# Optimization experiments

Measured on AMD Instinct MI355X. Metric: run time of the kernel, lower is better.

Reference implementation:

```python
import jax, jax.numpy as jnp
import numpy as np

EMBED_DIM = 512
NUM_HEADS = 8
HEAD_DIM = EMBED_DIM // NUM_HEADS
LN_EPS = 1e-5


def setup_inputs() -> dict:
    key = jax.random.key(0)
    ks = jax.random.split(key, 14)
    B, Lq, Lkv, E = 4, 1024, 4096, EMBED_DIM
    s = 0.02
    return {
        "query": jax.random.normal(ks[0], (B, Lq, E), dtype=jnp.float32),
        "key_value": jax.random.normal(ks[1], (B, Lkv, E), dtype=jnp.float32),
        "w_q": jax.random.normal(ks[2], (E, E), dtype=jnp.float32) * s,
        "w_k": jax.random.normal(ks[3], (E, E), dtype=jnp.float32) * s,
        "w_v": jax.random.normal(ks[4], (E, E), dtype=jnp.float32) * s,
        "b_q": jnp.zeros((E,), dtype=jnp.float32),
        "b_k": jnp.zeros((E,), dtype=jnp.float32),
        "b_v": jnp.zeros((E,), dtype=jnp.float32),
        "w_o": jax.random.normal(ks[5], (E, E), dtype=jnp.float32) * s,
        "b_o": jnp.zeros((E,), dtype=jnp.float32),
        "ln_gamma": jnp.ones((E,), dtype=jnp.float32),
        "ln_beta": jnp.zeros((E,), dtype=jnp.float32),
    }


def reference(query, key_value, w_q, w_k, w_v, b_q, b_k, b_v, w_o, b_o, ln_gamma, ln_beta):
    # query: [B, Lq, E]; key_value: [B, Lkv, E]
    B, Lq, E = query.shape
    Lkv = key_value.shape[1]
    H, D = NUM_HEADS, HEAD_DIM

    q = (query @ w_q.T + b_q).reshape(B, Lq, H, D)
    k = (key_value @ w_k.T + b_k).reshape(B, Lkv, H, D)
    v = (key_value @ w_v.T + b_v).reshape(B, Lkv, H, D)

    scale = 1.0 / jnp.sqrt(jnp.asarray(D, dtype=query.dtype))
    scores = jnp.einsum("bqhd,bkhd->bhqk", q, k) * scale  # [B,H,Lq,Lkv]
    attn = jax.nn.softmax(scores, axis=-1)
    # attn dropout off (eval mode)

    ctx = jnp.einsum("bhqk,bkhd->bqhd", attn, v).reshape(B, Lq, E)
    attn_output = ctx @ w_o.T + b_o
    # post-attn dropout off (eval mode)

    x = query + attn_output
    mu = jnp.mean(x, axis=-1, keepdims=True)
    var = jnp.mean(jnp.square(x - mu), axis=-1, keepdims=True)
    out = (x - mu) / jnp.sqrt(var + LN_EPS) * ln_gamma + ln_beta

    # need_weights=True: PyTorch averages attention weights over heads
    attn_weights = jnp.mean(attn, axis=1)  # [B, Lq, Lkv]
    return out, attn_weights
```

## Files before the change

### kernel.cpp

```cpp
#include <hip/hip_runtime.h>
#include <hip/hip_bf16.h>

namespace {

constexpr int E_DIM = 512;
constexpr int NH = 8;
constexpr int HD = 64;
constexpr int LQ = 1024;
constexpr int LKV = 4096;
constexpr int NB = 4;
constexpr int SPLIT = 4;
constexpr int SLICE = LKV / SPLIT;
constexpr int NT = SLICE / 64;
constexpr size_t CPL = (size_t)NB * LQ * E_DIM;

typedef __attribute__((ext_vector_type(8))) short bf16x8;
typedef __attribute__((ext_vector_type(8))) unsigned short u16x8;
typedef __attribute__((ext_vector_type(4))) float f32x4;

typedef const unsigned int __attribute__((address_space(1)))* gptr1;
typedef unsigned int __attribute__((address_space(3)))* lptr3;

__device__ __forceinline__ void gl16(const unsigned short* g, unsigned short* l) {
  __builtin_amdgcn_global_load_lds((gptr1)g, (lptr3)l, 16, 0, 0);
}

__device__ __forceinline__ f32x4 mfma16(bf16x8 a, bf16x8 b, f32x4 c) {
  return __builtin_amdgcn_mfma_f32_16x16x32_bf16(a, b, c, 0, 0, 0);
}

__device__ __forceinline__ unsigned short f2b(float f) {
  unsigned int u = __float_as_uint(f);
  u += 0x7FFFu + ((u >> 16) & 1u);
  return (unsigned short)(u >> 16);
}

__device__ __forceinline__ unsigned int cvt_pk_bf16(float a, float b) {
  unsigned int r;
  asm("v_cvt_pk_bf16_f32 %0, %1, %2" : "=v"(r) : "v"(a), "v"(b));
  return r;
}

__global__ __launch_bounds__(256) void cvt_all(
    const float* __restrict__ query, const float* __restrict__ kv,
    const float* __restrict__ w0, const float* __restrict__ w1,
    const float* __restrict__ w2, const float* __restrict__ w3,
    unsigned short* __restrict__ Qxb, unsigned short* __restrict__ KVb,
    unsigned short* __restrict__ Wb) {
  const int blk = blockIdx.x;
  const float* s;
  unsigned short* d;
  size_t idx;
  if (blk < 1024) {
    idx = ((size_t)blk * 256 + threadIdx.x) * 8;
    s = query; d = Qxb;
  } else if (blk < 5120) {
    idx = ((size_t)(blk - 1024) * 256 + threadIdx.x) * 8;
    s = kv; d = KVb;
  } else {
    idx = ((size_t)(blk - 5120) * 256 + threadIdx.x) * 8;
    const int widx = (int)(idx >> 18);
    s = widx == 0 ? w0 : widx == 1 ? w1 : widx == 2 ? w2 : w3;
    d = Wb;
    s -= (size_t)widx << 18;
  }
  const float4 a = *(const float4*)(s + idx);
  const float4 b = *(const float4*)(s + idx + 4);
  uint4 o;
  o.x = cvt_pk_bf16(a.x, a.y);
  o.y = cvt_pk_bf16(a.z, a.w);
  o.z = cvt_pk_bf16(b.x, b.y);
  o.w = cvt_pk_bf16(b.z, b.w);
  *(uint4*)(d + idx) = o;
}

template <int EPI>
__global__ __launch_bounds__(256) void gemm_bf16(
    const unsigned short* __restrict__ A, const unsigned short* __restrict__ B,
    const float* __restrict__ bias, void* __restrict__ outp, int L,
    float oscale) {
  __shared__ __align__(16) unsigned short As[128][32];
  __shared__ __align__(16) unsigned short Bs[128][32];
  const int tid = threadIdx.x;
  const int wv = tid >> 6, lane = tid & 63, lg = lane >> 4, lr = lane & 15;
  const int gx = gridDim.x, gy = gridDim.y;
  const int p = blockIdx.x + gx * blockIdx.y;
  const int xcd = p & 7, ii = p >> 3;
  const int by = xcd * (gy >> 3) + ii / gx;
  const int bx = ii - (ii / gx) * gx;
  const int i0 = by * 128, j0 = bx * 128;
  const int wm = wv >> 1, wn = wv & 1;
  const int srow = tid >> 2, scol = (tid & 3) * 8;
  f32x4 acc[4][4] = {};
  const unsigned short* ap = A + (size_t)(i0 + srow) * E_DIM + scol;
  const unsigned short* bp = B + (size_t)(j0 + srow) * E_DIM + scol;
  unsigned short* lA = &As[srow][scol];
  unsigned short* lB = &Bs[srow][scol];
  for (int k0 = 0; k0 < E_DIM; k0 += 32) {
    __syncthreads();
    gl16(ap + k0, lA);
    gl16(ap + k0 + (size_t)64 * E_DIM, lA + 64 * 32);
    gl16(bp + k0, lB);
    gl16(bp + k0 + (size_t)64 * E_DIM, lB + 64 * 32);
    __syncthreads();
    bf16x8 af[4], bg[4];
    for (int m = 0; m < 4; ++m)
      af[m] = *(const bf16x8*)&As[wm * 64 + m * 16 + lr][lg * 8];
    for (int n = 0; n < 4; ++n)
      bg[n] = *(const bf16x8*)&Bs[wn * 64 + n * 16 + lr][lg * 8];
    for (int m = 0; m < 4; ++m)
      for (int n = 0; n < 4; ++n)
        acc[m][n] = mfma16(af[m], bg[n], acc[m][n]);
  }
  for (int m = 0; m < 4; ++m)
    for (int n = 0; n < 4; ++n) {
      const int j = j0 + wn * 64 + n * 16 + lr;
      const float bj = bias[j];
      for (int r = 0; r < 4; ++r) {
        const int i = i0 + wm * 64 + m * 16 + lg * 4 + r;
        const float v = (acc[m][n][r] + bj) * oscale;
        if (EPI == 2) {
          ((float*)outp)[(size_t)i * E_DIM + j] = v;
        } else {
          const int bb = i / L, li = i - bb * L;
          const int hh = j >> 6, dd = j & 63;
          if (EPI == 0)
            ((unsigned short*)outp)[((size_t)(bb * NH + hh) * L + li) * HD + dd] = f2b(v);
          else
            ((unsigned short*)outp)[((size_t)(bb * NH + hh) * HD + dd) * L + li] = f2b(v);
        }
      }
    }
}

template <int EPI>
__global__ __launch_bounds__(256) void gemm64(
    const unsigned short* __restrict__ A, const unsigned short* __restrict__ B,
    const float* __restrict__ bias, void* __restrict__ outp, int L,
    float oscale) {
  __shared__ __align__(16) unsigned short As[64][32];
  __shared__ __align__(16) unsigned short Bs[128][32];
  const int tid = threadIdx.x;
  const int wv = tid >> 6, lane = tid & 63, lg = lane >> 4, lr = lane & 15;
  const int gx = gridDim.x, gy = gridDim.y;
  const int p = blockIdx.x + gx * blockIdx.y;
  const int xcd = p & 7, ii = p >> 3;
  const int by = xcd * (gy >> 3) + ii / gx;
  const int bx = ii - (ii / gx) * gx;
  const int i0 = by * 64, j0 = bx * 128;
  const int srow = tid >> 2, scol = (tid & 3) * 8;
  f32x4 acc[4][2] = {};
  const unsigned short* ap = A + (size_t)(i0 + srow) * E_DIM + scol;
  const unsigned short* bp = B + (size_t)(j0 + srow) * E_DIM + scol;
  unsigned short* lA = &As[srow][scol];
  unsigned short* lB = &Bs[srow][scol];
  for (int k0 = 0; k0 < E_DIM; k0 += 32) {
    __syncthreads();
    gl16(ap + k0, lA);
    gl16(bp + k0, lB);
    gl16(bp + k0 + (size_t)64 * E_DIM, lB + 64 * 32);
    __syncthreads();
    bf16x8 af[4], bg[2];
    for (int m = 0; m < 4; ++m)
      af[m] = *(const bf16x8*)&As[m * 16 + lr][lg * 8];
    for (int n = 0; n < 2; ++n)
      bg[n] = *(const bf16x8*)&Bs[wv * 32 + n * 16 + lr][lg * 8];
    for (int m = 0; m < 4; ++m)
      for (int n = 0; n < 2; ++n)
        acc[m][n] = mfma16(af[m], bg[n], acc[m][n]);
  }
  for (int m = 0; m < 4; ++m)
    for (int n = 0; n < 2; ++n) {
      const int j = j0 + wv * 32 + n * 16 + lr;
      const float bj = bias[j];
      for (int r = 0; r < 4; ++r) {
        const int i = i0 + m * 16 + lg * 4 + r;
        const float v = (acc[m][n][r] + bj) * oscale;
        if (EPI == 2) {
          ((float*)outp)[(size_t)i * E_DIM + j] = v;
        } else {
          const int bb = i / L, li = i - bb * L;
          const int hh = j >> 6, dd = j & 63;
          ((unsigned short*)outp)[((size_t)(bb * NH + hh) * L + li) * HD + dd] = f2b(v);
        }
      }
    }
}

__global__ __launch_bounds__(512) void attn_fused(
    const unsigned short* __restrict__ Qb, const unsigned short* __restrict__ Kb,
    const unsigned short* __restrict__ Vt, float* __restrict__ l_part,
    int* __restrict__ flags, float* __restrict__ attn_w,
    unsigned short* __restrict__ ctxp) {
  __shared__ __align__(16) unsigned short P[2][NH][64][64];
  const int tid = threadIdx.x;
  const int h = tid >> 6, lane = tid & 63, lg = lane >> 4, lr = lane & 15;
  const int p = blockIdx.x + 16 * blockIdx.y + 64 * blockIdx.z;
  const int xcd = p & 7, ii = p >> 3;
  const int combo = xcd * 2 + (ii >> 4);
  const int qg = ii & 15;
  const int q0 = qg * 64;
  const int b = combo >> 2, sp = combo & 3;
  const size_t bh = (size_t)b * NH + h;
  const unsigned short* Qp = Qb + (bh * LQ + q0) * HD;
  const unsigned short* Kp = Kb + (bh * LKV + sp * SLICE) * HD;
  const unsigned short* Vp = Vt + bh * HD * LKV + sp * SLICE;

  bf16x8 qB[4][2];
  for (int qs = 0; qs < 4; ++qs)
    for (int kk = 0; kk < 2; ++kk)
      qB[qs][kk] = *(const bf16x8*)(Qp + (qs * 16 + lr) * HD + kk * 32 + lg * 8);

  float qsum[4] = {};
  for (int t = 0; t < NT; ++t) {
    const unsigned short* base = Kp + (size_t)t * 64 * HD;
    for (int k2h = 0; k2h < 2; ++k2h) {
      bf16x8 kA[2][2];
      for (int k2 = 0; k2 < 2; ++k2)
        for (int kk = 0; kk < 2; ++kk)
          kA[k2][kk] = *(const bf16x8*)(base + ((k2h * 2 + k2) * 16 + lr) * HD +
                                        kk * 32 + lg * 8);
      f32x4 sacc[2][4] = {};
      for (int k2 = 0; k2 < 2; ++k2)
        for (int qs = 0; qs < 4; ++qs)
          sacc[k2][qs] = mfma16(kA[k2][1], qB[qs][1],
                                mfma16(kA[k2][0], qB[qs][0], sacc[k2][qs]));
      for (int k2 = 0; k2 < 2; ++k2)
        for (int qs = 0; qs < 4; ++qs)
          for (int r = 0; r < 4; ++r)
            qsum[qs] += __builtin_amdgcn_exp2f(sacc[k2][qs][r]);
    }
  }
  for (int qs = 0; qs < 4; ++qs) {
    float v = qsum[qs];
    v += __shfl_xor(v, 16);
    v += __shfl_xor(v, 32);
    if (lg == 0)
      l_part[(size_t)sp * (NB * NH * LQ) + bh * LQ + q0 + qs * 16 + lr] = v;
  }
  __syncthreads();
  if (tid == 0) {
    __threadfence();
    int* fl = &flags[b * 16 + qg];
    __hip_atomic_fetch_add(fl, 1, __ATOMIC_ACQ_REL, __HIP_MEMORY_SCOPE_AGENT);
    while (__hip_atomic_load(fl, __ATOMIC_ACQUIRE, __HIP_MEMORY_SCOPE_AGENT) < SPLIT) {
    }
    __threadfence();
  }
  __syncthreads();

  float nlg[4];
  for (int qs = 0; qs < 4; ++qs) {
    float ls = 0.f;
    for (int s = 0; s < SPLIT; ++s)
      ls += l_part[(size_t)s * (NB * NH * LQ) + bh * LQ + q0 + qs * 16 + lr];
    nlg[qs] = -__builtin_amdgcn_logf(ls) - 3.0f;
  }

  f32x4 cacc[4][4] = {};
  for (int t = 0; t < NT; ++t) {
    const int kv0 = t * 64;
    unsigned short (*Pb)[64][64] = P[t & 1];
    bf16x8 vf[4][2];
    for (int ds = 0; ds < 4; ++ds)
      for (int kk = 0; kk < 2; ++kk)
        vf[ds][kk] = *(const bf16x8*)(Vp + (size_t)(ds * 16 + lr) * LKV + kv0 +
                                      kk * 32 + lg * 8);
    for (int kh = 0; kh < 2; ++kh) {
      bf16x8 kA[2][2];
      for (int k2 = 0; k2 < 2; ++k2)
        for (int kk = 0; kk < 2; ++kk)
          kA[k2][kk] = *(const bf16x8*)(Kp + (size_t)(kv0 + (kh * 2 + k2) * 16 + lr) * HD +
                                        kk * 32 + lg * 8);
      f32x4 sacc[2][4] = {};
      for (int k2 = 0; k2 < 2; ++k2)
        for (int qs = 0; qs < 4; ++qs)
          sacc[k2][qs] = mfma16(kA[k2][1], qB[qs][1],
                                mfma16(kA[k2][0], qB[qs][0], sacc[k2][qs]));
      for (int k2 = 0; k2 < 2; ++k2)
        for (int qs = 0; qs < 4; ++qs) {
          const int q = qs * 16 + lr;
          const float p0 = __builtin_amdgcn_exp2f(sacc[k2][qs][0] + nlg[qs]);
          const float p1 = __builtin_amdgcn_exp2f(sacc[k2][qs][1] + nlg[qs]);
          const float p2 = __builtin_amdgcn_exp2f(sacc[k2][qs][2] + nlg[qs]);
          const float p3 = __builtin_amdgcn_exp2f(sacc[k2][qs][3] + nlg[qs]);
          uint2 w;
          w.x = cvt_pk_bf16(p0, p1);
          w.y = cvt_pk_bf16(p2, p3);
          const int col = ((kh * 2 + k2) * 16 + lg * 4) ^ ((q & 7) << 3);
          *(uint2*)&Pb[h][q][col] = w;
        }
    }
    for (int kk = 0; kk < 2; ++kk) {
      bf16x8 pa[4];
      for (int qs = 0; qs < 4; ++qs) {
        const int q = qs * 16 + lr;
        pa[qs] = *(const bf16x8*)&Pb[h][q][(kk * 32 + lg * 8) ^ ((q & 7) << 3)];
      }
      for (int qs = 0; qs < 4; ++qs)
        for (int ds = 0; ds < 4; ++ds)
          cacc[qs][ds] = mfma16(pa[qs], vf[ds][kk], cacc[qs][ds]);
    }
    __syncthreads();
    {
      const int qa = tid >> 3, La = tid & 7;
      const int col = (La * 8) ^ ((qa & 7) << 3);
      float2 s01 = {0.f, 0.f}, s23 = {0.f, 0.f}, s45 = {0.f, 0.f},
             s67 = {0.f, 0.f};
      for (int hh = 0; hh < NH; ++hh) {
        const uint4 v = *(const uint4*)&Pb[hh][qa][col];
        s01.x += __uint_as_float(v.x << 16);
        s01.y += __uint_as_float(v.x & 0xFFFF0000u);
        s23.x += __uint_as_float(v.y << 16);
        s23.y += __uint_as_float(v.y & 0xFFFF0000u);
        s45.x += __uint_as_float(v.z << 16);
        s45.y += __uint_as_float(v.z & 0xFFFF0000u);
        s67.x += __uint_as_float(v.w << 16);
        s67.y += __uint_as_float(v.w & 0xFFFF0000u);
      }
      float* op = attn_w + (size_t)(b * LQ + q0 + qa) * LKV + sp * SLICE + kv0 +
                  La * 8;
      float4 o0 = {s01.x, s01.y, s23.x, s23.y};
      float4 o1 = {s45.x, s45.y, s67.x, s67.y};
      *(float4*)op = o0;
      *(float4*)(op + 4) = o1;
    }
  }
  unsigned short* cp = ctxp + (size_t)sp * CPL;
  for (int qs = 0; qs < 4; ++qs)
    for (int ds = 0; ds < 4; ++ds)
      for (int r = 0; r < 4; ++r)
        cp[(size_t)(b * LQ + q0 + qs * 16 + lg * 4 + r) * E_DIM + h * HD +
           ds * 16 + lr] = f2b(cacc[qs][ds][r]);
}

__global__ __launch_bounds__(256) void combine_ctx(
    const unsigned short* __restrict__ ctxp, unsigned short* __restrict__ ctxb) {
  const size_t i = (size_t)blockIdx.x * 256 + threadIdx.x;
  float2 s01 = {0.f, 0.f}, s23 = {0.f, 0.f}, s45 = {0.f, 0.f}, s67 = {0.f, 0.f};
  for (int pl = 0; pl < SPLIT; ++pl) {
    const uint4 v = ((const uint4*)(ctxp + pl * CPL))[i];
    s01.x += __uint_as_float(v.x << 16);
    s01.y += __uint_as_float(v.x & 0xFFFF0000u);
    s23.x += __uint_as_float(v.y << 16);
    s23.y += __uint_as_float(v.y & 0xFFFF0000u);
    s45.x += __uint_as_float(v.z << 16);
    s45.y += __uint_as_float(v.z & 0xFFFF0000u);
    s67.x += __uint_as_float(v.w << 16);
    s67.y += __uint_as_float(v.w & 0xFFFF0000u);
  }
  uint4 o;
  o.x = cvt_pk_bf16(s01.x, s01.y);
  o.y = cvt_pk_bf16(s23.x, s23.y);
  o.z = cvt_pk_bf16(s45.x, s45.y);
  o.w = cvt_pk_bf16(s67.x, s67.y);
  ((uint4*)ctxb)[i] = o;
}

__global__ __launch_bounds__(256) void ln_kernel(
    const float* __restrict__ q, const float* __restrict__ ao,
    const float* __restrict__ gamma, const float* __restrict__ beta,
    float* __restrict__ out) {
  const int row = blockIdx.x;
  const int tid = threadIdx.x;
  const size_t base = (size_t)row * E_DIM;
  const float x0 = q[base + tid] + ao[base + tid];
  const float x1 = q[base + 256 + tid] + ao[base + 256 + tid];
  float s = x0 + x1, ss = x0 * x0 + x1 * x1;
  for (int off = 32; off >= 1; off >>= 1) {
    s += __shfl_down(s, off);
    ss += __shfl_down(ss, off);
  }
  __shared__ float ps[4], pss[4];
  if ((tid & 63) == 0) {
    ps[tid >> 6] = s;
    pss[tid >> 6] = ss;
  }
  __syncthreads();
  s = ps[0] + ps[1] + ps[2] + ps[3];
  ss = pss[0] + pss[1] + pss[2] + pss[3];
  const float mu = s * (1.f / E_DIM);
  float var = ss * (1.f / E_DIM) - mu * mu;
  var = fmaxf(var, 0.f);
  const float rstd = rsqrtf(var + 1e-5f);
  out[base + tid] = (x0 - mu) * rstd * gamma[tid] + beta[tid];
  out[base + 256 + tid] = (x1 - mu) * rstd * gamma[256 + tid] + beta[256 + tid];
}

}

extern "C" void kernel_launch(void* const* d_in, const int* in_sizes, int n_in,
                              void* d_out, int out_size, void* d_ws, size_t ws_size,
                              hipStream_t stream) {
  const float* query = (const float*)d_in[0];
  const float* key_value = (const float*)d_in[1];
  const float* w_q = (const float*)d_in[2];
  const float* w_k = (const float*)d_in[3];
  const float* w_v = (const float*)d_in[4];
  const float* b_q = (const float*)d_in[5];
  const float* b_k = (const float*)d_in[6];
  const float* b_v = (const float*)d_in[7];
  const float* w_o = (const float*)d_in[8];
  const float* b_o = (const float*)d_in[9];
  const float* ln_g = (const float*)d_in[10];
  const float* ln_b = (const float*)d_in[11];

  unsigned short* Qb = (unsigned short*)d_ws;
  unsigned short* Kb = Qb + (size_t)2097152;
  unsigned short* Vt = Kb + (size_t)8388608;
  float* l_part = (float*)(Vt + (size_t)8388608);
  int* flags = (int*)(l_part + (size_t)SPLIT * NB * NH * LQ);
  unsigned short* Wb = (unsigned short*)(l_part + 262144);
  float* ao = (float*)(Wb + 1048576);
  unsigned short* KVb = (unsigned short*)(ao + 2097152);
  unsigned short* Qxb = KVb + (size_t)8388608;
  unsigned short* ctxp = KVb;
  unsigned short* ctxb = Qb;

  float* out = (float*)d_out;
  float* attn_w = out + (size_t)NB * LQ * E_DIM;

  const float qscale = 0.125f * 1.44269504088896340736f;

  hipMemsetAsync(flags, 0, sizeof(int) * NB * 16, stream);

  cvt_all<<<dim3(5632), dim3(256), 0, stream>>>(query, key_value, w_q, w_k, w_v,
                                                w_o, Qxb, KVb, Wb);

  gemm64<0><<<dim3(4, 64), dim3(256), 0, stream>>>(Qxb, Wb, b_q, Qb, LQ, qscale);
  gemm_bf16<0><<<dim3(4, 128), dim3(256), 0, stream>>>(KVb, Wb + 262144, b_k, Kb,
                                                       LKV, 1.0f);
  gemm_bf16<1><<<dim3(4, 128), dim3(256), 0, stream>>>(KVb, Wb + 524288, b_v, Vt,
                                                       LKV, 8.0f);

  attn_fused<<<dim3(16, NB, SPLIT), dim3(512), 0, stream>>>(Qb, Kb, Vt, l_part,
                                                            flags, attn_w, ctxp);
  combine_ctx<<<dim3(1024), dim3(256), 0, stream>>>(ctxp, ctxb);
  gemm64<2><<<dim3(4, 64), dim3(256), 0, stream>>>(ctxb, Wb + 786432, b_o, ao,
                                                   LQ, 1.0f);
  ln_kernel<<<dim3(NB * LQ), dim3(256), 0, stream>>>(query, ao, ln_g, ln_b, out);
}
```

Measured before the change: 215.3 us.

## Merge QKV projections into one launch and fold ctx split-combine into output GEMM

The three Q/K/V projection GEMMs become a single launch with a z-dimension selecting the projection. Blocks for Q return early when blockIdx.y is 64 or above. The separate combine_ctx kernel is removed: the output-projection GEMM now sums the four split-KV partial context slices while loading its A tile, then writes the bf16 result to shared memory. This saves two kernel launches and one round trip of the combined context through global memory. In exchange, the A-tile loads become synchronous register loads rather than global_load_lds, and some launched blocks do no work.

```diff
diff --git a/kernel.cpp b/kernel.cpp
--- a/kernel.cpp
+++ b/kernel.cpp
@@ -33,6 +33,10 @@
   unsigned int u = __float_as_uint(f);
   u += 0x7FFFu + ((u >> 16) & 1u);
   return (unsigned short)(u >> 16);
+}
+
+__device__ __forceinline__ float b2f(short s) {
+  return __uint_as_float(((unsigned int)(unsigned short)s) << 16);
 }
 
 __device__ __forceinline__ unsigned int cvt_pk_bf16(float a, float b) {
@@ -74,26 +78,71 @@
   *(uint4*)(d + idx) = o;
 }
 
-template <int EPI>
-__global__ __launch_bounds__(256) void gemm_bf16(
-    const unsigned short* __restrict__ A, const unsigned short* __restrict__ B,
-    const float* __restrict__ bias, void* __restrict__ outp, int L,
-    float oscale) {
+__global__ __launch_bounds__(256) void proj_qkv(
+    const unsigned short* __restrict__ Qxb, const unsigned short* __restrict__ KVb,
+    const unsigned short* __restrict__ Wb, const float* __restrict__ b_q,
+    const float* __restrict__ b_k, const float* __restrict__ b_v,
+    unsigned short* __restrict__ Qb, unsigned short* __restrict__ Kb,
+    unsigned short* __restrict__ Vt, float qscale) {
   __shared__ __align__(16) unsigned short As[128][32];
   __shared__ __align__(16) unsigned short Bs[128][32];
   const int tid = threadIdx.x;
   const int wv = tid >> 6, lane = tid & 63, lg = lane >> 4, lr = lane & 15;
-  const int gx = gridDim.x, gy = gridDim.y;
-  const int p = blockIdx.x + gx * blockIdx.y;
+  const int srow = tid >> 2, scol = (tid & 3) * 8;
+  const int z = blockIdx.z;
+
+  if (z == 0) {
+    if (blockIdx.y >= 64) return;
+    const int p = blockIdx.x + 4 * blockIdx.y;
+    const int xcd = p & 7, ii = p >> 3;
+    const int by = xcd * 8 + ii / 4;
+    const int bx = ii - (ii / 4) * 4;
+    const int i0 = by * 64, j0 = bx * 128;
+    f32x4 acc[4][2] = {};
+    const unsigned short* ap = Qxb + (size_t)(i0 + srow) * E_DIM + scol;
+    const unsigned short* bp = Wb + (size_t)(j0 + srow) * E_DIM + scol;
+    unsigned short* lA = &As[srow][scol];
+    unsigned short* lB = &Bs[srow][scol];
+    for (int k0 = 0; k0 < E_DIM; k0 += 32) {
+      __syncthreads();
+      gl16(ap + k0, lA);
+      gl16(bp + k0, lB);
+      gl16(bp + k0 + (size_t)64 * E_DIM, lB + 64 * 32);
+      __syncthreads();
+      bf16x8 af[4], bg[2];
+      for (int m = 0; m < 4; ++m)
+        af[m] = *(const bf16x8*)&As[m * 16 + lr][lg * 8];
+      for (int n = 0; n < 2; ++n)
+        bg[n] = *(const bf16x8*)&Bs[wv * 32 + n * 16 + lr][lg * 8];
+      for (int m = 0; m < 4; ++m)
+        for (int n = 0; n < 2; ++n)
+          acc[m][n] = mfma16(af[m], bg[n], acc[m][n]);
+    }
+    for (int m = 0; m < 4; ++m)
+      for (int n = 0; n < 2; ++n) {
+        const int j = j0 + wv * 32 + n * 16 + lr;
+        const float bj = b_q[j];
+        const int hh = j >> 6, dd = j & 63;
+        for (int r = 0; r < 4; ++r) {
+          const int i = i0 + m * 16 + lg * 4 + r;
+          const int bb = i / LQ, li = i - bb * LQ;
+          Qb[((size_t)(bb * NH + hh) * LQ + li) * HD + dd] =
+              f2b((acc[m][n][r] + bj) * qscale);
+        }
+      }
+    return;
+  }
+
+  const int p = blockIdx.x + 4 * blockIdx.y;
   const int xcd = p & 7, ii = p >> 3;
-  const int by = xcd * (gy >> 3) + ii / gx;
-  const int bx = ii - (ii / gx) * gx;
+  const int by = xcd * 16 + ii / 4;
+  const int bx = ii - (ii / 4) * 4;
   const int i0 = by * 128, j0 = bx * 128;
   const int wm = wv >> 1, wn = wv & 1;
-  const int srow = tid >> 2, scol = (tid & 3) * 8;
   f32x4 acc[4][4] = {};
-  const unsigned short* ap = A + (size_t)(i0 + srow) * E_DIM + scol;
-  const unsigned short* bp = B + (size_t)(j0 + srow) * E_DIM + scol;
+  const unsigned short* ap = KVb + (size_t)(i0 + srow) * E_DIM + scol;
+  const unsigned short* bp = (z == 1 ? Wb + 262144 : Wb + 524288) +
+                             (size_t)(j0 + srow) * E_DIM + scol;
   unsigned short* lA = &As[srow][scol];
   unsigned short* lB = &Bs[srow][scol];
   for (int k0 = 0; k0 < E_DIM; k0 += 32) {
@@ -112,77 +161,20 @@
       for (int n = 0; n < 4; ++n)
         acc[m][n] = mfma16(af[m], bg[n], acc[m][n]);
   }
+  const float* bias = (z == 1) ? b_k : b_v;
   for (int m = 0; m < 4; ++m)
     for (int n = 0; n < 4; ++n) {
       const int j = j0 + wn * 64 + n * 16 + lr;
       const float bj = bias[j];
+      const int hh = j >> 6, dd = j & 63;
       for (int r = 0; r < 4; ++r) {
         const int i = i0 + wm * 64 + m * 16 + lg * 4 + r;
-        const float v = (acc[m][n][r] + bj) * oscale;
-        if (EPI == 2) {
-          ((float*)outp)[(size_t)i * E_DIM + j] = v;
-        } else {
-          const int bb = i / L, li = i - bb * L;
-          const int hh = j >> 6, dd = j & 63;
-          if (EPI == 0)
-            ((unsigned short*)outp)[((size_t)(bb * NH + hh) * L + li) * HD + dd] = f2b(v);
-          else
-            ((unsigned short*)outp)[((size_t)(bb * NH + hh) * HD + dd) * L + li] = f2b(v);
-        }
-      }
-    }
-}
-
-template <int EPI>
-__global__ __launch_bounds__(256) void gemm64(
-    const unsigned short* __restrict__ A, const unsigned short* __restrict__ B,
-    const float* __restrict__ bias, void* __restrict__ outp, int L,
-    float oscale) {
-  __shared__ __align__(16) unsigned short As[64][32];
-  __shared__ __align__(16) unsigned short Bs[128][32];
-  const int tid = threadIdx.x;
-  const int wv = tid >> 6, lane = tid & 63, lg = lane >> 4, lr = lane & 15;
-  const int gx = gridDim.x, gy = gridDim.y;
-  const int p = blockIdx.x + gx * blockIdx.y;
-  const int xcd = p & 7, ii = p >> 3;
-  const int by = xcd * (gy >> 3) + ii / gx;
-  const int bx = ii - (ii / gx) * gx;
-  const int i0 = by * 64, j0 = bx * 128;
-  const int srow = tid >> 2, scol = (tid & 3) * 8;
-  f32x4 acc[4][2] = {};
-  const unsigned short* ap = A + (size_t)(i0 + srow) * E_DIM + scol;
-  const unsigned short* bp = B + (size_t)(j0 + srow) * E_DIM + scol;
-  unsigned short* lA = &As[srow][scol];
-  unsigned short* lB = &Bs[srow][scol];
-  for (int k0 = 0; k0 < E_DIM; k0 += 32) {
-    __syncthreads();
-    gl16(ap + k0, lA);
-    gl16(bp + k0, lB);
-    gl16(bp + k0 + (size_t)64 * E_DIM, lB + 64 * 32);
-    __syncthreads();
-    bf16x8 af[4], bg[2];
-    for (int m = 0; m < 4; ++m)
-      af[m] = *(const bf16x8*)&As[m * 16 + lr][lg * 8];
-    for (int n = 0; n < 2; ++n)
-      bg[n] = *(const bf16x8*)&Bs[wv * 32 + n * 16 + lr][lg * 8];
-    for (int m = 0; m < 4; ++m)
-      for (int n = 0; n < 2; ++n)
-        acc[m][n] = mfma16(af[m], bg[n], acc[m][n]);
-  }
-  for (int m = 0; m < 4; ++m)
-    for (int n = 0; n < 2; ++n) {
-      const int j = j0 + wv * 32 + n * 16 + lr;
-      const float bj = bias[j];
-      for (int r = 0; r < 4; ++r) {
-        const int i = i0 + m * 16 + lg * 4 + r;
-        const float v = (acc[m][n][r] + bj) * oscale;
-        if (EPI == 2) {
-          ((float*)outp)[(size_t)i * E_DIM + j] = v;
-        } else {
-          const int bb = i / L, li = i - bb * L;
-          const int hh = j >> 6, dd = j & 63;
-          ((unsigned short*)outp)[((size_t)(bb * NH + hh) * L + li) * HD + dd] = f2b(v);
-        }
+        const int bb = i / LKV, li = i - bb * LKV;
+        if (z == 1)
+          Kb[((size_t)(bb * NH + hh) * LKV + li) * HD + dd] = f2b(acc[m][n][r] + bj);
+        else
+          Vt[((size_t)(bb * NH + hh) * HD + dd) * LKV + li] =
+              f2b((acc[m][n][r] + bj) * 8.0f);
       }
     }
 }
@@ -334,27 +326,58 @@
            ds * 16 + lr] = f2b(cacc[qs][ds][r]);
 }
 
-__global__ __launch_bounds__(256) void combine_ctx(
-    const unsigned short* __restrict__ ctxp, unsigned short* __restrict__ ctxb) {
-  const size_t i = (size_t)blockIdx.x * 256 + threadIdx.x;
-  float2 s01 = {0.f, 0.f}, s23 = {0.f, 0.f}, s45 = {0.f, 0.f}, s67 = {0.f, 0.f};
-  for (int pl = 0; pl < SPLIT; ++pl) {
-    const uint4 v = ((const uint4*)(ctxp + pl * CPL))[i];
-    s01.x += __uint_as_float(v.x << 16);
-    s01.y += __uint_as_float(v.x & 0xFFFF0000u);
-    s23.x += __uint_as_float(v.y << 16);
-    s23.y += __uint_as_float(v.y & 0xFFFF0000u);
-    s45.x += __uint_as_float(v.z << 16);
-    s45.y += __uint_as_float(v.z & 0xFFFF0000u);
-    s67.x += __uint_as_float(v.w << 16);
-    s67.y += __uint_as_float(v.w & 0xFFFF0000u);
-  }
-  uint4 o;
-  o.x = cvt_pk_bf16(s01.x, s01.y);
-  o.y = cvt_pk_bf16(s23.x, s23.y);
-  o.z = cvt_pk_bf16(s45.x, s45.y);
-  o.w = cvt_pk_bf16(s67.x, s67.y);
-  ((uint4*)ctxb)[i] = o;
+__global__ __launch_bounds__(256) void gemm_o(
+    const unsigned short* __restrict__ ctxp, const unsigned short* __restrict__ B,
+    const float* __restrict__ bias, float* __restrict__ outp) {
+  __shared__ __align__(16) unsigned short As[64][32];
+  __shared__ __align__(16) unsigned short Bs[128][32];
+  const int tid = threadIdx.x;
+  const int wv = tid >> 6, lane = tid & 63, lg = lane >> 4, lr = lane & 15;
+  const int p = blockIdx.x + 4 * blockIdx.y;
+  const int xcd = p & 7, ii = p >> 3;
+  const int by = xcd * 8 + ii / 4;
+  const int bx = ii - (ii / 4) * 4;
+  const int i0 = by * 64, j0 = bx * 128;
+  const int srow = tid >> 2, scol = (tid & 3) * 8;
+  f32x4 acc[4][2] = {};
+  const unsigned short* ap = ctxp + (size_t)(i0 + srow) * E_DIM + scol;
+  const unsigned short* bp = B + (size_t)(j0 + srow) * E_DIM + scol;
+  unsigned short* lB = &Bs[srow][scol];
+  for (int k0 = 0; k0 < E_DIM; k0 += 32) {
+    float s[8] = {};
+#pragma unroll
+    for (int pl = 0; pl < 4; ++pl) {
+      const u16x8 v = *(const u16x8*)(ap + (size_t)pl * CPL + k0);
+      for (int j = 0; j < 8; ++j) s[j] += b2f((short)v[j]);
+    }
+    __syncthreads();
+    gl16(bp + k0, lB);
+    gl16(bp + k0 + (size_t)64 * E_DIM, lB + 64 * 32);
+    uint4 o;
+    o.x = cvt_pk_bf16(s[0], s[1]);
+    o.y = cvt_pk_bf16(s[2], s[3]);
+    o.z = cvt_pk_bf16(s[4], s[5]);
+    o.w = cvt_pk_bf16(s[6], s[7]);
+    *(uint4*)&As[srow & 63][scol] = o;
+    __syncthreads();
+    bf16x8 af[4], bg[2];
+    for (int m = 0; m < 4; ++m)
+      af[m] = *(const bf16x8*)&As[m * 16 + lr][lg * 8];
+    for (int n = 0; n < 2; ++n)
+      bg[n] = *(const bf16x8*)&Bs[wv * 32 + n * 16 + lr][lg * 8];
+    for (int m = 0; m < 4; ++m)
+      for (int n = 0; n < 2; ++n)
+        acc[m][n] = mfma16(af[m], bg[n], acc[m][n]);
+  }
+  for (int m = 0; m < 4; ++m)
+    for (int n = 0; n < 2; ++n) {
+      const int j = j0 + wv * 32 + n * 16 + lr;
+      const float bj = bias[j];
+      for (int r = 0; r < 4; ++r) {
+        const int i = i0 + m * 16 + lg * 4 + r;
+        outp[(size_t)i * E_DIM + j] = acc[m][n][r] + bj;
+      }
+    }
 }
 
 __global__ __launch_bounds__(256) void ln_kernel(
@@ -415,7 +438,6 @@
   unsigned short* KVb = (unsigned short*)(ao + 2097152);
   unsigned short* Qxb = KVb + (size_t)8388608;
   unsigned short* ctxp = KVb;
-  unsigned short* ctxb = Qb;
 
   float* out = (float*)d_out;
   float* attn_w = out + (size_t)NB * LQ * E_DIM;
@@ -427,16 +449,11 @@
   cvt_all<<<dim3(5632), dim3(256), 0, stream>>>(query, key_value, w_q, w_k, w_v,
                                                 w_o, Qxb, KVb, Wb);
 
-  gemm64<0><<<dim3(4, 64), dim3(256), 0, stream>>>(Qxb, Wb, b_q, Qb, LQ, qscale);
-  gemm_bf16<0><<<dim3(4, 128), dim3(256), 0, stream>>>(KVb, Wb + 262144, b_k, Kb,
-                                                       LKV, 1.0f);
-  gemm_bf16<1><<<dim3(4, 128), dim3(256), 0, stream>>>(KVb, Wb + 524288, b_v, Vt,
-                                                       LKV, 8.0f);
+  proj_qkv<<<dim3(4, 128, 3), dim3(256), 0, stream>>>(Qxb, KVb, Wb, b_q, b_k,
+                                                      b_v, Qb, Kb, Vt, qscale);
 
   attn_fused<<<dim3(16, NB, SPLIT), dim3(512), 0, stream>>>(Qb, Kb, Vt, l_part,
                                                             flags, attn_w, ctxp);
-  combine_ctx<<<dim3(1024), dim3(256), 0, stream>>>(ctxp, ctxb);
-  gemm64<2><<<dim3(4, 64), dim3(256), 0, stream>>>(ctxb, Wb + 786432, b_o, ao,
-                                                   LQ, 1.0f);
+  gemm_o<<<dim3(4, 64), dim3(256), 0, stream>>>(ctxp, Wb + 786432, b_o, ao);
   ln_kernel<<<dim3(NB * LQ), dim3(256), 0, stream>>>(query, ao, ln_g, ln_b, out);
 }
```

Result: slower. 447.8 us (+108.0%).
